# Performance work log

Measured on AMD Instinct MI355X. Metric: run time of the kernel, lower is better.

The kernel has to match this reference:

```python
import jax, jax.numpy as jnp
import numpy as np

EMBED = 768
HEADS = 12
HEAD_DIM = EMBED // HEADS
HIDDEN = 4 * EMBED
EPS = 1e-5


def _layernorm(x, g, b):
    mu = jnp.mean(x, axis=-1, keepdims=True)
    var = jnp.var(x, axis=-1, keepdims=True)
    return (x - mu) * jax.lax.rsqrt(var + EPS) * g + b


def setup_inputs() -> dict:
    key = jax.random.key(0)
    ks = jax.random.split(key, 12)
    s_e = 1.0 / np.sqrt(EMBED)
    s_h = 1.0 / np.sqrt(HIDDEN)
    return {
        "x": jax.random.normal(ks[0], (2, 2048, EMBED), dtype=jnp.float32),
        "ln1_g": jnp.ones((EMBED,), jnp.float32),
        "ln1_b": jnp.zeros((EMBED,), jnp.float32),
        "qkv_w": jax.random.uniform(ks[1], (EMBED, 3 * EMBED), jnp.float32, -s_e, s_e),
        "qkv_b": jax.random.uniform(ks[2], (3 * EMBED,), jnp.float32, -s_e, s_e),
        "proj_w": jax.random.uniform(ks[3], (EMBED, EMBED), jnp.float32, -s_e, s_e),
        "proj_b": jax.random.uniform(ks[4], (EMBED,), jnp.float32, -s_e, s_e),
        "ln2_g": jnp.ones((EMBED,), jnp.float32),
        "ln2_b": jnp.zeros((EMBED,), jnp.float32),
        "fc1_w": jax.random.uniform(ks[5], (EMBED, HIDDEN), jnp.float32, -s_e, s_e),
        "fc1_b": jax.random.uniform(ks[6], (HIDDEN,), jnp.float32, -s_e, s_e),
        "fc2_w": jax.random.uniform(ks[7], (HIDDEN, EMBED), jnp.float32, -s_h, s_h),
        "fc2_b": jax.random.uniform(ks[8], (EMBED,), jnp.float32, -s_h, s_h),
    }


def reference(x, ln1_g, ln1_b, qkv_w, qkv_b, proj_w, proj_b,
              ln2_g, ln2_b, fc1_w, fc1_b, fc2_w, fc2_b):
    B, L, C = x.shape
    scale = HEAD_DIM ** -0.5

    # --- attention sublayer (pre-LN) ---
    h = _layernorm(x, ln1_g, ln1_b)
    qkv = h @ qkv_w + qkv_b                       # [B, L, 3C]
    qkv = qkv.reshape(B, L, 3, HEADS, HEAD_DIM)
    q = jnp.transpose(qkv[:, :, 0], (0, 2, 1, 3))  # [B, H, L, D]
    k = jnp.transpose(qkv[:, :, 1], (0, 2, 1, 3))
    v = jnp.transpose(qkv[:, :, 2], (0, 2, 1, 3))
    attn = jnp.einsum('bhqd,bhkd->bhqk', q, k) * scale  # [B, H, L, L]
    attn = jax.nn.softmax(attn, axis=-1)
    out = jnp.einsum('bhqk,bhkd->bhqd', attn, v)  # [B, H, L, D]
    out = jnp.transpose(out, (0, 2, 1, 3)).reshape(B, L, C)
    x = x + (out @ proj_w + proj_b)

    # --- FFN sublayer (pre-LN) ---
    h = _layernorm(x, ln2_g, ln2_b)
    h = jax.nn.gelu(h @ fc1_w + fc1_b, approximate=False)
    x = x + (h @ fc2_w + fc2_b)
    return x
```

## Files before the change

kernel.cpp:

```cpp
#include <hip/hip_runtime.h>
#include <hip/hip_bf16.h>
#include <math.h>

#define EMBED   768
#define NHEADS  12
#define HD      64
#define HIDDEN  3072
#define SEQ     2048
#define BATCH   2
#define ROWS    (BATCH*SEQ)

#define QSCALE  0.1803368801111204f

typedef __bf16 bf16_t;
typedef __attribute__((ext_vector_type(8))) __bf16 bf16x8;
typedef __attribute__((ext_vector_type(4))) float f32x4;

static __device__ __forceinline__ f32x4 mfma16(bf16x8 a, bf16x8 b, f32x4 c) {
  return __builtin_amdgcn_mfma_f32_16x16x32_bf16(a, b, c, 0, 0, 0);
}

typedef __attribute__((address_space(1))) const void gas_void;
typedef __attribute__((address_space(3))) void las_void;
static __device__ __forceinline__ void gll16(const void* g, void* l) {
  __builtin_amdgcn_global_load_lds((gas_void*)g, (las_void*)l, 16, 0, 0);
}

__global__ __launch_bounds__(256) void ln_kernel(
    const float* __restrict__ x, const float* __restrict__ g,
    const float* __restrict__ bt, bf16_t* __restrict__ out)
{
  int row = blockIdx.x;
  int tid = threadIdx.x;
  const float* xr = x + (size_t)row * EMBED;
  float v0 = xr[tid], v1 = xr[tid + 256], v2 = xr[tid + 512];
  float s  = v0 + v1 + v2;
  float s2 = v0*v0 + v1*v1 + v2*v2;
  #pragma unroll
  for (int o = 32; o >= 1; o >>= 1) {
    s  += __shfl_xor(s,  o, 64);
    s2 += __shfl_xor(s2, o, 64);
  }
  __shared__ float red[8];
  int wave = tid >> 6, lane = tid & 63;
  if (lane == 0) { red[wave] = s; red[wave + 4] = s2; }
  __syncthreads();
  s  = red[0] + red[1] + red[2] + red[3];
  s2 = red[4] + red[5] + red[6] + red[7];
  float mu  = s * (1.0f / EMBED);
  float var = s2 * (1.0f / EMBED) - mu * mu;
  float rs  = rsqrtf(var + 1e-5f);
  bf16_t* orow = out + (size_t)row * EMBED;
  orow[tid]       = (bf16_t)((v0 - mu) * rs * g[tid]       + bt[tid]);
  orow[tid + 256] = (bf16_t)((v1 - mu) * rs * g[tid + 256] + bt[tid + 256]);
  orow[tid + 512] = (bf16_t)((v2 - mu) * rs * g[tid + 512] + bt[tid + 512]);
}

__global__ __launch_bounds__(256) void transpose_cast(
    const float* __restrict__ in, bf16_t* __restrict__ out, int R, int C)
{
  __shared__ float tile[32][33];
  int c0 = blockIdx.x * 32, r0 = blockIdx.y * 32;
  int tx = threadIdx.x & 31, ty = threadIdx.x >> 5;
  #pragma unroll
  for (int p = 0; p < 4; ++p) {
    int r = ty + p * 8;
    tile[r][tx] = in[(size_t)(r0 + r) * C + c0 + tx];
  }
  __syncthreads();
  #pragma unroll
  for (int p = 0; p < 4; ++p) {
    int cc = ty + p * 8;
    out[(size_t)(c0 + cc) * R + r0 + tx] = (bf16_t)tile[tx][cc];
  }
}

__global__ __launch_bounds__(256) void v_transpose(
    const bf16_t* __restrict__ qkv, bf16_t* __restrict__ vt)
{
  __shared__ bf16_t tile[64][68];
  int bh = blockIdx.y;
  int b = bh / NHEADS, h = bh % NHEADS;
  int l0 = blockIdx.x * 64;
  int t = threadIdx.x;
  int dx = (t & 15) * 4;
  int ly = t >> 4;
  #pragma unroll
  for (int p = 0; p < 4; ++p) {
    int l = ly + p * 16;
    const bf16_t* src = qkv + (size_t)(b * SEQ + l0 + l) * 2304 + 1536 + h * HD + dx;
    *(uint2*)&tile[l][dx] = *(const uint2*)src;
  }
  __syncthreads();
  int lx = (t & 15) * 4;
  int dy = t >> 4;
  #pragma unroll
  for (int p = 0; p < 4; ++p) {
    int d = dy + p * 16;
    union { bf16_t h4[4]; uint2 u; } tmp;
    #pragma unroll
    for (int i = 0; i < 4; ++i) tmp.h4[i] = tile[lx + i][d];
    *(uint2*)&vt[((size_t)bh * HD + d) * SEQ + l0 + lx] = tmp.u;
  }
}

template<int MODE, int BN>
__global__ __launch_bounds__(256) void gemm_kernel(
    const bf16_t* __restrict__ A, const bf16_t* __restrict__ WT,
    const float* __restrict__ bias, const float* __restrict__ res,
    void* __restrict__ outp, int N, int K)
{
  constexpr int JT = BN / 32;
  __shared__ bf16_t As[128 * 64];
  __shared__ bf16_t Bs[BN * 64];
  int tid = threadIdx.x;
  int lane = tid & 63, wave = tid >> 6;
  int l15 = lane & 15, quad = lane >> 4;
  int wm = wave >> 1, wn = wave & 1;
  int m0 = blockIdx.y * 128, n0 = blockIdx.x * BN;

  f32x4 acc[4][JT];
  #pragma unroll
  for (int i = 0; i < 4; ++i)
    #pragma unroll
    for (int j = 0; j < JT; ++j)
      acc[i][j] = (f32x4){0.f, 0.f, 0.f, 0.f};

  int grow = lane >> 3;
  int gcol = ((lane & 7) ^ grow) * 8;
  const bf16_t* abase = A  + (size_t)(m0 + wave * 32 + grow) * K + gcol;
  const bf16_t* bbase = WT + (size_t)(n0 + wave * (BN / 4) + grow) * K + gcol;
  int swk = l15 & 7;

  for (int k0 = 0; k0 < K; k0 += 64) {
    #pragma unroll
    for (int a = 0; a < 4; ++a)
      gll16(abase + (size_t)a * 8 * K + k0, &As[(wave * 32 + a * 8) * 64]);
    #pragma unroll
    for (int a = 0; a < BN / 32; ++a)
      gll16(bbase + (size_t)a * 8 * K + k0, &Bs[(wave * (BN / 4) + a * 8) * 64]);
    __syncthreads();

    #pragma unroll
    for (int g = 0; g < 2; ++g) {
      bf16x8 af[4], bfr[JT];
      #pragma unroll
      for (int i = 0; i < 4; ++i)
        af[i] = *(const bf16x8*)
            &As[(wm * 64 + i * 16 + l15) * 64 + (((g * 4 + quad) ^ swk) * 8)];
      #pragma unroll
      for (int j = 0; j < JT; ++j)
        bfr[j] = *(const bf16x8*)
            &Bs[(wn * (BN / 2) + j * 16 + l15) * 64 + (((g * 4 + quad) ^ swk) * 8)];
      #pragma unroll
      for (int i = 0; i < 4; ++i)
        #pragma unroll
        for (int j = 0; j < JT; ++j)
          acc[i][j] = mfma16(af[i], bfr[j], acc[i][j]);
    }
    __syncthreads();
  }

  #pragma unroll
  for (int i = 0; i < 4; ++i) {
    int mbase = m0 + wm * 64 + i * 16 + quad * 4;
    #pragma unroll
    for (int j = 0; j < JT; ++j) {
      int n = n0 + wn * (BN / 2) + j * 16 + l15;
      float bn = bias[n];
      #pragma unroll
      for (int r = 0; r < 4; ++r) {
        size_t idx = (size_t)(mbase + r) * N + n;
        float v = acc[i][j][r] + bn;
        if (MODE == 1) v = 0.5f * v * (1.0f + erff(v * 0.70710678118654752f));
        if (MODE == 3 && n < 768) v *= QSCALE;
        if (MODE == 2) {
          v += res[idx];
          ((float*)outp)[idx] = v;
        } else {
          ((bf16_t*)outp)[idx] = (bf16_t)v;
        }
      }
    }
  }
}

__global__ __launch_bounds__(256, 3) void attn_kernel(
    const bf16_t* __restrict__ qkv, const bf16_t* __restrict__ vt,
    bf16_t* __restrict__ attnout)
{
  __attribute__((aligned(16))) __shared__ bf16_t smem[8192 + 8192 + 10240];
  __shared__ float dsumf[4][64];

  int qt = blockIdx.x, h = blockIdx.y, b = blockIdx.z;
  int tid = threadIdx.x;
  int wave = tid >> 6, lane = tid & 63;
  int l15 = lane & 15, quad = lane >> 4;
  int q0 = qt * 64;
  int bh = b * NHEADS + h;

  bf16_t* kt  = smem + wave * 2048;
  bf16_t* vtl = smem + 8192 + wave * 2048;
  bf16_t* pt  = smem + 16384 + wave * 2560;

  bf16x8 aq[4][2];
  #pragma unroll
  for (int qi = 0; qi < 4; ++qi) {
    const bf16_t* qrow = qkv + (size_t)(b * SEQ + q0 + qi * 16 + l15) * 2304
                             + h * HD + quad * 8;
    aq[qi][0] = *(const bf16x8*)qrow;
    aq[qi][1] = *(const bf16x8*)(qrow + 32);
  }

  f32x4 accO[4][4];
  #pragma unroll
  for (int qi = 0; qi < 4; ++qi)
    #pragma unroll
    for (int t2 = 0; t2 < 4; ++t2)
      accO[qi][t2] = (f32x4){0.f, 0.f, 0.f, 0.f};
  float lpart[4][4] = {};

  int krow_l = lane >> 3;
  int kchunk = ((lane & 7) ^ krow_l) * 8;
  const bf16_t* ksrc0 = qkv + (size_t)(b * SEQ + wave * 32 + krow_l) * 2304
                            + 768 + h * HD + kchunk;
  int vrow_l = lane >> 2;
  int vchunk = ((lane & 3) ^ (vrow_l & 3)) * 8;
  const bf16_t* vsrc0 = vt + ((size_t)bh * HD + vrow_l) * SEQ + wave * 32 + vchunk;
  int swk = l15 & 7, swv = l15 & 3;

  for (int kv0 = 0; kv0 < SEQ; kv0 += 128) {
    const bf16_t* ks = ksrc0 + (size_t)kv0 * 2304;
    gll16(ks,                       kt);
    gll16(ks + (size_t) 8 * 2304,   kt + 512);
    gll16(ks + (size_t)16 * 2304,   kt + 1024);
    gll16(ks + (size_t)24 * 2304,   kt + 1536);
    const bf16_t* vs = vsrc0 + kv0;
    gll16(vs,                       vtl);
    gll16(vs + (size_t)16 * SEQ,    vtl + 512);
    gll16(vs + (size_t)32 * SEQ,    vtl + 1024);
    gll16(vs + (size_t)48 * SEQ,    vtl + 1536);
    __asm__ volatile("s_waitcnt vmcnt(0)" ::: "memory");

    bf16x8 bk[2][2];
    #pragma unroll
    for (int t = 0; t < 2; ++t)
      #pragma unroll
      for (int f = 0; f < 2; ++f)
        bk[t][f] = *(const bf16x8*)
            &kt[(t * 16 + l15) * 64 + (((f * 4 + quad) ^ swk) * 8)];

    #pragma unroll
    for (int qi = 0; qi < 4; ++qi) {
      #pragma unroll
      for (int t = 0; t < 2; ++t) {
        f32x4 s = (f32x4){0.f, 0.f, 0.f, 0.f};
        s = mfma16(aq[qi][0], bk[t][0], s);
        s = mfma16(aq[qi][1], bk[t][1], s);
        #pragma unroll
        for (int r = 0; r < 4; ++r) {
          float pv = exp2f(s[r]);
          lpart[qi][r] += pv;
          pt[(qi * 16 + quad * 4 + r) * 40 + t * 16 + l15] = (bf16_t)pv;
        }
      }
    }

    #pragma unroll
    for (int qi = 0; qi < 4; ++qi) {
      bf16x8 ap = *(const bf16x8*)&pt[(qi * 16 + l15) * 40 + quad * 8];
      #pragma unroll
      for (int t2 = 0; t2 < 4; ++t2) {
        bf16x8 bv = *(const bf16x8*)
            &vtl[(t2 * 16 + l15) * 32 + ((quad ^ swv) * 8)];
        accO[qi][t2] = mfma16(ap, bv, accO[qi][t2]);
      }
    }
  }

  #pragma unroll
  for (int qi = 0; qi < 4; ++qi)
    #pragma unroll
    for (int r = 0; r < 4; ++r) {
      float l = lpart[qi][r];
      l += __shfl_xor(l, 1, 64);
      l += __shfl_xor(l, 2, 64);
      l += __shfl_xor(l, 4, 64);
      l += __shfl_xor(l, 8, 64);
      lpart[qi][r] = l;
    }
  if (l15 == 0) {
    #pragma unroll
    for (int qi = 0; qi < 4; ++qi)
      #pragma unroll
      for (int r = 0; r < 4; ++r)
        dsumf[wave][qi * 16 + quad * 4 + r] = lpart[qi][r];
  }
  __syncthreads();

  float* slabf = (float*)smem;
  int rq = lane >> 3;
  int d0 = (lane & 7) * 8;

  #pragma unroll
  for (int pass = 0; pass < 2; ++pass) {
    if (pass) __syncthreads();
    #pragma unroll
    for (int qi2 = 0; qi2 < 2; ++qi2) {
      int qi = pass * 2 + qi2;
      #pragma unroll
      for (int t2 = 0; t2 < 4; ++t2)
        #pragma unroll
        for (int r = 0; r < 4; ++r)
          slabf[wave * 2048 + (qi2 * 16 + quad * 4 + r) * 64 + t2 * 16 + l15]
              = accO[qi][t2][r];
    }
    __syncthreads();
    int q_loc = wave * 8 + rq;
    f32x4 o0 = (f32x4){0.f,0.f,0.f,0.f}, o1 = (f32x4){0.f,0.f,0.f,0.f};
    #pragma unroll
    for (int sw = 0; sw < 4; ++sw) {
      o0 += *(const f32x4*)&slabf[sw * 2048 + q_loc * 64 + d0];
      o1 += *(const f32x4*)&slabf[sw * 2048 + q_loc * 64 + d0 + 4];
    }
    int q_abs = pass * 32 + q_loc;
    float den = dsumf[0][q_abs] + dsumf[1][q_abs] + dsumf[2][q_abs] + dsumf[3][q_abs];
    float inv = 1.0f / den;
    bf16_t ob[8];
    #pragma unroll
    for (int j = 0; j < 4; ++j) {
      ob[j]     = (bf16_t)(o0[j] * inv);
      ob[j + 4] = (bf16_t)(o1[j] * inv);
    }
    *(uint4*)&attnout[(size_t)(b * SEQ + q0 + q_abs) * EMBED + h * HD + d0]
        = *(const uint4*)ob;
  }
}

extern "C" void kernel_launch(void* const* d_in, const int* in_sizes, int n_in,
                              void* d_out, int out_size, void* d_ws, size_t ws_size,
                              hipStream_t stream) {
  (void)in_sizes; (void)n_in; (void)out_size; (void)ws_size;
  const float* x      = (const float*)d_in[0];
  const float* ln1_g  = (const float*)d_in[1];
  const float* ln1_b  = (const float*)d_in[2];
  const float* qkv_w  = (const float*)d_in[3];
  const float* qkv_b  = (const float*)d_in[4];
  const float* proj_w = (const float*)d_in[5];
  const float* proj_b = (const float*)d_in[6];
  const float* ln2_g  = (const float*)d_in[7];
  const float* ln2_b  = (const float*)d_in[8];
  const float* fc1_w  = (const float*)d_in[9];
  const float* fc1_b  = (const float*)d_in[10];
  const float* fc2_w  = (const float*)d_in[11];
  const float* fc2_b  = (const float*)d_in[12];
  float* out = (float*)d_out;

  char* p = (char*)d_ws;
  bf16_t* wqkvT  = (bf16_t*)p; p += (size_t)2304 * 768 * 2;
  bf16_t* wprojT = (bf16_t*)p; p += (size_t)768 * 768 * 2;
  bf16_t* wfc1T  = (bf16_t*)p; p += (size_t)3072 * 768 * 2;
  bf16_t* wfc2T  = (bf16_t*)p; p += (size_t)768 * 3072 * 2;
  bf16_t* hbuf   = (bf16_t*)p; p += (size_t)ROWS * 768 * 2;
  bf16_t* qkv    = (bf16_t*)p;
  bf16_t* hid    = (bf16_t*)p; p += (size_t)ROWS * 3072 * 2;
  bf16_t* vt     = (bf16_t*)p; p += (size_t)BATCH * NHEADS * HD * SEQ * 2;
  bf16_t* attno  = (bf16_t*)p; p += (size_t)ROWS * 768 * 2;

  transpose_cast<<<dim3(2304/32, 768/32),  256, 0, stream>>>(qkv_w,  wqkvT,  768,  2304);
  transpose_cast<<<dim3(768/32,  768/32),  256, 0, stream>>>(proj_w, wprojT, 768,  768);
  transpose_cast<<<dim3(3072/32, 768/32),  256, 0, stream>>>(fc1_w,  wfc1T,  768,  3072);
  transpose_cast<<<dim3(768/32,  3072/32), 256, 0, stream>>>(fc2_w,  wfc2T,  3072, 768);

  ln_kernel<<<ROWS, 256, 0, stream>>>(x, ln1_g, ln1_b, hbuf);
  gemm_kernel<3,128><<<dim3(2304/128, ROWS/128), 256, 0, stream>>>(
      hbuf, wqkvT, qkv_b, nullptr, qkv, 2304, 768);
  v_transpose<<<dim3(SEQ/64, BATCH*NHEADS), 256, 0, stream>>>(qkv, vt);
  attn_kernel<<<dim3(SEQ/64, NHEADS, BATCH), 256, 0, stream>>>(qkv, vt, attno);
  gemm_kernel<2,64><<<dim3(768/64, ROWS/128), 256, 0, stream>>>(
      attno, wprojT, proj_b, x, out, 768, 768);

  ln_kernel<<<ROWS, 256, 0, stream>>>(out, ln2_g, ln2_b, hbuf);
  gemm_kernel<1,128><<<dim3(3072/128, ROWS/128), 256, 0, stream>>>(
      hbuf, wfc1T, fc1_b, nullptr, hid, 3072, 768);
  gemm_kernel<2,64><<<dim3(768/64, ROWS/128), 256, 0, stream>>>(
      hid, wfc2T, fc2_b, out, out, 768, 3072);
}
```

Measured before the change: 311.0 us.

## Compute transposed scores so P stays in registers, drop LDS staging of K/V

The attention kernel now computes S^T by swapping MFMA operands (K as A, Q as B). Each lane's score fragment then directly matches the B-operand layout of a 16x16x16 bf16 MFMA, so P is packed into registers and fed to the PV product without writing to LDS. K and V are loaded directly from global memory into registers, replacing the global_load_lds staging and its vmcnt wait. Row sums are reduced across quads with two shuffles instead of four. The trade-off is uncoalesced per-lane global loads, which lean on the cache, plus twice as many smaller-K MFMAs for PV.

```diff
diff --git a/kernel.cpp b/kernel.cpp
--- a/kernel.cpp
+++ b/kernel.cpp
@@ -15,10 +15,23 @@
 typedef __bf16 bf16_t;
 typedef __attribute__((ext_vector_type(8))) __bf16 bf16x8;
 typedef __attribute__((ext_vector_type(4))) float f32x4;
+typedef __attribute__((ext_vector_type(4))) short short4v;
 
 static __device__ __forceinline__ f32x4 mfma16(bf16x8 a, bf16x8 b, f32x4 c) {
   return __builtin_amdgcn_mfma_f32_16x16x32_bf16(a, b, c, 0, 0, 0);
 }
+
+#if __has_builtin(__builtin_amdgcn_mfma_f32_16x16x16bf16_1k)
+#define HAVE_X16 1
+static __device__ __forceinline__ f32x4 mfma16k16(short4v a, short4v b, f32x4 c) {
+  return __builtin_amdgcn_mfma_f32_16x16x16bf16_1k(a, b, c, 0, 0, 0);
+}
+#elif __has_builtin(__builtin_amdgcn_mfma_f32_16x16x16_bf16)
+#define HAVE_X16 1
+static __device__ __forceinline__ f32x4 mfma16k16(short4v a, short4v b, f32x4 c) {
+  return __builtin_amdgcn_mfma_f32_16x16x16_bf16(a, b, c, 0, 0, 0);
+}
+#endif
 
 typedef __attribute__((address_space(1))) const void gas_void;
 typedef __attribute__((address_space(3))) void las_void;
@@ -189,8 +202,11 @@
     const bf16_t* __restrict__ qkv, const bf16_t* __restrict__ vt,
     bf16_t* __restrict__ attnout)
 {
-  __attribute__((aligned(16))) __shared__ bf16_t smem[8192 + 8192 + 10240];
+  __shared__ float slabf[4 * 2048];
   __shared__ float dsumf[4][64];
+#ifndef HAVE_X16
+  __shared__ bf16_t ptile[4][16 * 40 * 4];
+#endif
 
   int qt = blockIdx.x, h = blockIdx.y, b = blockIdx.z;
   int tid = threadIdx.x;
@@ -199,17 +215,13 @@
   int q0 = qt * 64;
   int bh = b * NHEADS + h;
 
-  bf16_t* kt  = smem + wave * 2048;
-  bf16_t* vtl = smem + 8192 + wave * 2048;
-  bf16_t* pt  = smem + 16384 + wave * 2560;
-
-  bf16x8 aq[4][2];
+  bf16x8 bq[4][2];
   #pragma unroll
   for (int qi = 0; qi < 4; ++qi) {
     const bf16_t* qrow = qkv + (size_t)(b * SEQ + q0 + qi * 16 + l15) * 2304
                              + h * HD + quad * 8;
-    aq[qi][0] = *(const bf16x8*)qrow;
-    aq[qi][1] = *(const bf16x8*)(qrow + 32);
+    bq[qi][0] = *(const bf16x8*)qrow;
+    bq[qi][1] = *(const bf16x8*)(qrow + 32);
   }
 
   f32x4 accO[4][4];
@@ -218,87 +230,90 @@
     #pragma unroll
     for (int t2 = 0; t2 < 4; ++t2)
       accO[qi][t2] = (f32x4){0.f, 0.f, 0.f, 0.f};
-  float lpart[4][4] = {};
-
-  int krow_l = lane >> 3;
-  int kchunk = ((lane & 7) ^ krow_l) * 8;
-  const bf16_t* ksrc0 = qkv + (size_t)(b * SEQ + wave * 32 + krow_l) * 2304
-                            + 768 + h * HD + kchunk;
-  int vrow_l = lane >> 2;
-  int vchunk = ((lane & 3) ^ (vrow_l & 3)) * 8;
-  const bf16_t* vsrc0 = vt + ((size_t)bh * HD + vrow_l) * SEQ + wave * 32 + vchunk;
-  int swk = l15 & 7, swv = l15 & 3;
+  float lpart[4] = {0.f, 0.f, 0.f, 0.f};
+
+  const bf16_t* kb = qkv + (size_t)(b * SEQ + wave * 32 + l15) * 2304
+                         + 768 + h * HD + quad * 8;
+  const bf16_t* vb = vt + ((size_t)bh * HD + l15) * SEQ + wave * 32 + quad * 4;
 
   for (int kv0 = 0; kv0 < SEQ; kv0 += 128) {
-    const bf16_t* ks = ksrc0 + (size_t)kv0 * 2304;
-    gll16(ks,                       kt);
-    gll16(ks + (size_t) 8 * 2304,   kt + 512);
-    gll16(ks + (size_t)16 * 2304,   kt + 1024);
-    gll16(ks + (size_t)24 * 2304,   kt + 1536);
-    const bf16_t* vs = vsrc0 + kv0;
-    gll16(vs,                       vtl);
-    gll16(vs + (size_t)16 * SEQ,    vtl + 512);
-    gll16(vs + (size_t)32 * SEQ,    vtl + 1024);
-    gll16(vs + (size_t)48 * SEQ,    vtl + 1536);
-    __asm__ volatile("s_waitcnt vmcnt(0)" ::: "memory");
-
-    bf16x8 bk[2][2];
-    #pragma unroll
-    for (int t = 0; t < 2; ++t)
-      #pragma unroll
-      for (int f = 0; f < 2; ++f)
-        bk[t][f] = *(const bf16x8*)
-            &kt[(t * 16 + l15) * 64 + (((f * 4 + quad) ^ swk) * 8)];
+    bf16x8 ak[2][2];
+    #pragma unroll
+    for (int t = 0; t < 2; ++t) {
+      const bf16_t* kr = kb + (size_t)(kv0 + t * 16) * 2304;
+      ak[t][0] = *(const bf16x8*)kr;
+      ak[t][1] = *(const bf16x8*)(kr + 32);
+    }
+#ifdef HAVE_X16
+    short4v bv[4][2];
+    #pragma unroll
+    for (int t2 = 0; t2 < 4; ++t2)
+      #pragma unroll
+      for (int t = 0; t < 2; ++t)
+        bv[t2][t] = *(const short4v*)(vb + (size_t)t2 * 16 * SEQ + kv0 + t * 16);
 
     #pragma unroll
     for (int qi = 0; qi < 4; ++qi) {
+      short4v pk[2];
       #pragma unroll
       for (int t = 0; t < 2; ++t) {
         f32x4 s = (f32x4){0.f, 0.f, 0.f, 0.f};
-        s = mfma16(aq[qi][0], bk[t][0], s);
-        s = mfma16(aq[qi][1], bk[t][1], s);
+        s = mfma16(ak[t][0], bq[qi][0], s);
+        s = mfma16(ak[t][1], bq[qi][1], s);
+        union { bf16_t b4[4]; short4v s4; } u;
+        float ls = 0.f;
         #pragma unroll
         for (int r = 0; r < 4; ++r) {
           float pv = exp2f(s[r]);
-          lpart[qi][r] += pv;
-          pt[(qi * 16 + quad * 4 + r) * 40 + t * 16 + l15] = (bf16_t)pv;
+          ls += pv;
+          u.b4[r] = (bf16_t)pv;
+        }
+        lpart[qi] += ls;
+        pk[t] = u.s4;
+      }
+      #pragma unroll
+      for (int t2 = 0; t2 < 4; ++t2) {
+        accO[qi][t2] = mfma16k16(pk[0], bv[t2][0], accO[qi][t2]);
+        accO[qi][t2] = mfma16k16(pk[1], bv[t2][1], accO[qi][t2]);
+      }
+    }
+#else
+    bf16x8 bv32[4];
+    #pragma unroll
+    for (int t2 = 0; t2 < 4; ++t2)
+      bv32[t2] = *(const bf16x8*)(vt + ((size_t)bh * HD + t2 * 16 + l15) * SEQ
+                                  + wave * 32 + kv0 + quad * 8);
+    #pragma unroll
+    for (int qi = 0; qi < 4; ++qi) {
+      #pragma unroll
+      for (int t = 0; t < 2; ++t) {
+        f32x4 s = (f32x4){0.f, 0.f, 0.f, 0.f};
+        s = mfma16(ak[t][0], bq[qi][0], s);
+        s = mfma16(ak[t][1], bq[qi][1], s);
+        #pragma unroll
+        for (int r = 0; r < 4; ++r) {
+          float pv = exp2f(s[r]);
+          lpart[qi] += pv;
+          ptile[wave][(qi * 16 + l15) * 40 + t * 16 + quad * 4 + r] = (bf16_t)pv;
         }
       }
-    }
-
-    #pragma unroll
-    for (int qi = 0; qi < 4; ++qi) {
-      bf16x8 ap = *(const bf16x8*)&pt[(qi * 16 + l15) * 40 + quad * 8];
-      #pragma unroll
-      for (int t2 = 0; t2 < 4; ++t2) {
-        bf16x8 bv = *(const bf16x8*)
-            &vtl[(t2 * 16 + l15) * 32 + ((quad ^ swv) * 8)];
-        accO[qi][t2] = mfma16(ap, bv, accO[qi][t2]);
-      }
-    }
-  }
-
-  #pragma unroll
-  for (int qi = 0; qi < 4; ++qi)
-    #pragma unroll
-    for (int r = 0; r < 4; ++r) {
-      float l = lpart[qi][r];
-      l += __shfl_xor(l, 1, 64);
-      l += __shfl_xor(l, 2, 64);
-      l += __shfl_xor(l, 4, 64);
-      l += __shfl_xor(l, 8, 64);
-      lpart[qi][r] = l;
-    }
-  if (l15 == 0) {
-    #pragma unroll
-    for (int qi = 0; qi < 4; ++qi)
-      #pragma unroll
-      for (int r = 0; r < 4; ++r)
-        dsumf[wave][qi * 16 + quad * 4 + r] = lpart[qi][r];
+      bf16x8 ap = *(const bf16x8*)&ptile[wave][(qi * 16 + l15) * 40 + quad * 8];
+      #pragma unroll
+      for (int t2 = 0; t2 < 4; ++t2)
+        accO[qi][t2] = mfma16(ap, bv32[t2], accO[qi][t2]);
+    }
+#endif
+  }
+
+  #pragma unroll
+  for (int qi = 0; qi < 4; ++qi) {
+    float l = lpart[qi];
+    l += __shfl_xor(l, 16, 64);
+    l += __shfl_xor(l, 32, 64);
+    if (quad == 0) dsumf[wave][qi * 16 + l15] = l;
   }
   __syncthreads();
 
-  float* slabf = (float*)smem;
   int rq = lane >> 3;
   int d0 = (lane & 7) * 8;
 
```

Result: slower. 326.0 us (+4.8%).
